# Performance work log

Measured on AMD Instinct MI355X. Metric: run time of the kernel, lower is better.

## Reference

```python
import jax, jax.numpy as jnp
import numpy as np

B, N, D = 64, 2048, 64
KC = 512
BETA = 0.5


def setup_inputs() -> dict:
    key = jax.random.key(0)
    k1, k2, k3 = jax.random.split(key, 3)
    F_active = jax.random.normal(k1, (B, N, D), dtype=jnp.float32)
    centers = jax.random.normal(k2, (KC, D), dtype=jnp.float32)
    psi = 0.1 * jax.random.normal(k3, (KC,), dtype=jnp.float32)
    beta = jnp.float32(BETA)
    return {"F_active": F_active, "centers": centers, "psi": psi, "beta": beta}


def reference(F_active, centers, psi, beta):
    # Squared Euclidean distance via GEMM expansion (avoids the (B,N,Kc,d) diff tensor):
    # ||f - c||^2 = ||f||^2 + ||c||^2 - 2 f.c
    f2 = jnp.sum(F_active * F_active, axis=-1, keepdims=True)          # (B, N, 1)
    c2 = jnp.sum(centers * centers, axis=-1)                           # (Kc,)
    fc = jnp.einsum('bnd,kd->bnk', F_active, centers)                  # (B, N, Kc)
    dist2 = jnp.maximum(f2 + c2[None, None, :] - 2.0 * fc, 0.0)       # (B, N, Kc)
    sim = jnp.exp(-beta * dist2)                                       # (B, N, Kc)
    w = jax.nn.softmax(psi, axis=0)                                    # (Kc,)
    score_per_slot = jnp.einsum('bnk,k->bn', sim, w)                   # (B, N)
    return jnp.mean(score_per_slot, axis=1)                            # (B,)
```

## Files before the change

### kernel.cpp

```cpp
#include <hip/hip_runtime.h>

typedef _Float16 f16x8 __attribute__((ext_vector_type(8)));
typedef float f32x4 __attribute__((ext_vector_type(4)));

static constexpr float kLog2e = 1.44269504088896340736f;

#define WS_E2 65536
#define WS_W  (65536 + 2048)
#define WS_SC (65536 + 4096)

__device__ __forceinline__ float fast_exp2(float x) {
#if __has_builtin(__builtin_amdgcn_exp2f)
  return __builtin_amdgcn_exp2f(x);
#else
  return exp2f(x);
#endif
}

__global__ __launch_bounds__(512) void prep_kernel(
    const float* __restrict__ centers, const float* __restrict__ psi,
    const float* __restrict__ beta, float* __restrict__ e2,
    float* __restrict__ w, float* __restrict__ sc) {
  __shared__ float red[8];
  const int tid = threadIdx.x;
  const int lane = tid & 63;
  const int wid = tid >> 6;
  const float b = beta[0];
  const float kco = -b * kLog2e;

  const float4* crow = (const float4*)(centers + tid * 64);
  float c2 = 0.f;
#pragma unroll
  for (int i = 0; i < 16; ++i) {
    const float4 v = crow[i];
    c2 = fmaf(v.x, v.x, c2); c2 = fmaf(v.y, v.y, c2);
    c2 = fmaf(v.z, v.z, c2); c2 = fmaf(v.w, v.w, c2);
  }

  const float p = psi[tid];
  float m = p;
#pragma unroll
  for (int d = 1; d < 64; d <<= 1) m = fmaxf(m, __shfl_xor(m, d, 64));
  if (lane == 0) red[wid] = m;
  __syncthreads();
  float mx = red[0];
#pragma unroll
  for (int i = 1; i < 8; ++i) mx = fmaxf(mx, red[i]);
  __syncthreads();
  const float ex = fast_exp2((p - mx) * kLog2e);
  float ssum = ex;
#pragma unroll
  for (int d = 1; d < 64; d <<= 1) ssum += __shfl_xor(ssum, d, 64);
  if (lane == 0) red[wid] = ssum;
  __syncthreads();
  float tot = 0.f;
#pragma unroll
  for (int i = 0; i < 8; ++i) tot += red[i];

  w[tid] = ex / tot;
  e2[tid] = kco * c2;
  if (tid == 0) { sc[0] = 2.f * b * kLog2e; sc[1] = kco; }
}

__global__ __launch_bounds__(64) void cfrag_kernel(
    const float* __restrict__ centers, _Float16* __restrict__ cfrag) {
  const int idx = blockIdx.x * 64 + threadIdx.x;
  const int lane = idx & 63;
  const int pair = idx >> 6;
  const int t = pair >> 1;
  const int kk = pair & 1;
  const int n = t * 16 + (lane & 15);
  const int k = kk * 32 + (lane >> 4) * 8;
  const float* src = centers + n * 64 + k;
  const float4 v0 = *(const float4*)(src);
  const float4 v1 = *(const float4*)(src + 4);
  f16x8 h;
  h[0] = (_Float16)v0.x; h[1] = (_Float16)v0.y;
  h[2] = (_Float16)v0.z; h[3] = (_Float16)v0.w;
  h[4] = (_Float16)v1.x; h[5] = (_Float16)v1.y;
  h[6] = (_Float16)v1.z; h[7] = (_Float16)v1.w;
  *(f16x8*)(cfrag + (size_t)idx * 8) = h;
}

__global__ __launch_bounds__(256, 4) void score_kernel(
    const float* __restrict__ F, const _Float16* __restrict__ cfrag,
    const float* __restrict__ e2, const float* __restrict__ wgt,
    const float* __restrict__ sc, float* __restrict__ out) {
  __shared__ float f2s[128];
  __shared__ float wsum[4];
  const int tid = threadIdx.x;
  const int lane = tid & 63;
  const int wv = tid >> 6;
  const int quad = lane >> 4;
  const int l15 = lane & 15;
  const int R0 = blockIdx.x * 128;

  const float cC = sc[0];
  const float kco = sc[1];

  f16x8 a[2][2];
#pragma unroll
  for (int rt = 0; rt < 2; ++rt) {
    const int row = R0 + wv * 32 + rt * 16 + l15;
    const float* fr = F + row * 64 + quad * 8;
    float ssq = 0.f;
#pragma unroll
    for (int kk = 0; kk < 2; ++kk) {
      const float4 v0 = *(const float4*)(fr + kk * 32);
      const float4 v1 = *(const float4*)(fr + kk * 32 + 4);
      a[rt][kk][0] = (_Float16)v0.x; a[rt][kk][1] = (_Float16)v0.y;
      a[rt][kk][2] = (_Float16)v0.z; a[rt][kk][3] = (_Float16)v0.w;
      a[rt][kk][4] = (_Float16)v1.x; a[rt][kk][5] = (_Float16)v1.y;
      a[rt][kk][6] = (_Float16)v1.z; a[rt][kk][7] = (_Float16)v1.w;
      ssq = fmaf(v0.x, v0.x, ssq); ssq = fmaf(v0.y, v0.y, ssq);
      ssq = fmaf(v0.z, v0.z, ssq); ssq = fmaf(v0.w, v0.w, ssq);
      ssq = fmaf(v1.x, v1.x, ssq); ssq = fmaf(v1.y, v1.y, ssq);
      ssq = fmaf(v1.z, v1.z, ssq); ssq = fmaf(v1.w, v1.w, ssq);
    }
    ssq += __shfl_xor(ssq, 16, 64);
    ssq += __shfl_xor(ssq, 32, 64);
    if (quad == 0) f2s[wv * 32 + rt * 16 + l15] = ssq;
  }
  __syncthreads();

  float p0[2][4];
#pragma unroll
  for (int rt = 0; rt < 2; ++rt)
#pragma unroll
    for (int r = 0; r < 4; ++r)
      p0[rt][r] = kco * f2s[wv * 32 + rt * 16 + quad * 4 + r];

  float s = 0.f;
  for (int t = 0; t < 32; ++t) {
    const f16x8 b0 = *(const f16x8*)(cfrag + (size_t)((t * 2 + 0) * 64 + lane) * 8);
    const f16x8 b1 = *(const f16x8*)(cfrag + (size_t)((t * 2 + 1) * 64 + lane) * 8);
    const float e2v = e2[t * 16 + l15];
    const float wv2 = wgt[t * 16 + l15];
    f32x4 acc0 = {0.f, 0.f, 0.f, 0.f};
    f32x4 acc1 = {0.f, 0.f, 0.f, 0.f};
    acc0 = __builtin_amdgcn_mfma_f32_16x16x32_f16(a[0][0], b0, acc0, 0, 0, 0);
    acc0 = __builtin_amdgcn_mfma_f32_16x16x32_f16(a[0][1], b1, acc0, 0, 0, 0);
    acc1 = __builtin_amdgcn_mfma_f32_16x16x32_f16(a[1][0], b0, acc1, 0, 0, 0);
    acc1 = __builtin_amdgcn_mfma_f32_16x16x32_f16(a[1][1], b1, acc1, 0, 0, 0);
    float esum = 0.f;
#pragma unroll
    for (int r = 0; r < 4; ++r) {
      const float arg0 = fminf(fmaf(acc0[r], cC, p0[0][r] + e2v), 0.f);
      const float arg1 = fminf(fmaf(acc1[r], cC, p0[1][r] + e2v), 0.f);
      esum += fast_exp2(arg0);
      esum += fast_exp2(arg1);
    }
    s = fmaf(wv2, esum, s);
  }

#pragma unroll
  for (int d = 1; d < 64; d <<= 1) s += __shfl_xor(s, d, 64);
  if (lane == 0) wsum[wv] = s;
  __syncthreads();
  if (tid == 0) {
    const float tot = wsum[0] + wsum[1] + wsum[2] + wsum[3];
    atomicAdd(out + (blockIdx.x >> 4), tot * (1.0f / 2048.0f));
  }
}

extern "C" void kernel_launch(void* const* d_in, const int* in_sizes, int n_in,
                              void* d_out, int out_size, void* d_ws, size_t ws_size,
                              hipStream_t stream) {
  const float* F = (const float*)d_in[0];
  const float* centers = (const float*)d_in[1];
  const float* psi = (const float*)d_in[2];
  const float* beta = (const float*)d_in[3];
  float* out = (float*)d_out;
  char* ws = (char*)d_ws;
  _Float16* cfrag = (_Float16*)ws;
  float* e2 = (float*)(ws + WS_E2);
  float* wgt = (float*)(ws + WS_W);
  float* sc = (float*)(ws + WS_SC);

  hipMemsetAsync(out, 0, out_size * sizeof(float), stream);
  prep_kernel<<<1, 512, 0, stream>>>(centers, psi, beta, e2, wgt, sc);
  cfrag_kernel<<<64, 64, 0, stream>>>(centers, cfrag);
  score_kernel<<<1024, 256, 0, stream>>>(F, cfrag, e2, wgt, sc, out);
}
```

Baseline: 104.3 us.

## Fuse prep, fragment and memset launches; fold bias and scale into MFMA

Folds the center fp16 fragment packing and the output zeroing into the single prep kernel. This removes a kernel launch and a memset. The score kernel now pre-scales F by 2*beta*log2e before the fp16 conversion and seeds the MFMA accumulator with the bias terms, which removes per-element FMAs from the exp loop. The e2 and weight values are packed into one float2 load, and the loop is unrolled by 2. Scaling before the fp16 cast slightly changes rounding, and the prep kernel's cfrag writes from a single block are less coalesced.

```diff
diff --git a/kernel.cpp b/kernel.cpp
--- a/kernel.cpp
+++ b/kernel.cpp
@@ -5,9 +5,7 @@
 
 static constexpr float kLog2e = 1.44269504088896340736f;
 
-#define WS_E2 65536
-#define WS_W  (65536 + 2048)
-#define WS_SC (65536 + 4096)
+#define WS_EW 65536
 
 __device__ __forceinline__ float fast_exp2(float x) {
 #if __has_builtin(__builtin_amdgcn_exp2f)
@@ -19,25 +17,26 @@
 
 __global__ __launch_bounds__(512) void prep_kernel(
     const float* __restrict__ centers, const float* __restrict__ psi,
-    const float* __restrict__ beta, float* __restrict__ e2,
-    float* __restrict__ w, float* __restrict__ sc) {
+    const float* __restrict__ beta, _Float16* __restrict__ cfrag,
+    float2* __restrict__ ew, float* __restrict__ out) {
   __shared__ float red[8];
-  const int tid = threadIdx.x;
-  const int lane = tid & 63;
-  const int wid = tid >> 6;
+  const int n = threadIdx.x;
+  const int lane = n & 63;
+  const int wid = n >> 6;
   const float b = beta[0];
   const float kco = -b * kLog2e;
 
-  const float4* crow = (const float4*)(centers + tid * 64);
+  float4 row[16];
+  const float4* crow = (const float4*)(centers + n * 64);
   float c2 = 0.f;
 #pragma unroll
   for (int i = 0; i < 16; ++i) {
-    const float4 v = crow[i];
-    c2 = fmaf(v.x, v.x, c2); c2 = fmaf(v.y, v.y, c2);
-    c2 = fmaf(v.z, v.z, c2); c2 = fmaf(v.w, v.w, c2);
+    row[i] = crow[i];
+    c2 = fmaf(row[i].x, row[i].x, c2); c2 = fmaf(row[i].y, row[i].y, c2);
+    c2 = fmaf(row[i].z, row[i].z, c2); c2 = fmaf(row[i].w, row[i].w, c2);
   }
 
-  const float p = psi[tid];
+  const float p = psi[n];
   float m = p;
 #pragma unroll
   for (int d = 1; d < 64; d <<= 1) m = fmaxf(m, __shfl_xor(m, d, 64));
@@ -57,35 +56,33 @@
 #pragma unroll
   for (int i = 0; i < 8; ++i) tot += red[i];
 
-  w[tid] = ex / tot;
-  e2[tid] = kco * c2;
-  if (tid == 0) { sc[0] = 2.f * b * kLog2e; sc[1] = kco; }
-}
+  ew[n] = make_float2(kco * c2, ex / tot);
 
-__global__ __launch_bounds__(64) void cfrag_kernel(
-    const float* __restrict__ centers, _Float16* __restrict__ cfrag) {
-  const int idx = blockIdx.x * 64 + threadIdx.x;
-  const int lane = idx & 63;
-  const int pair = idx >> 6;
-  const int t = pair >> 1;
-  const int kk = pair & 1;
-  const int n = t * 16 + (lane & 15);
-  const int k = kk * 32 + (lane >> 4) * 8;
-  const float* src = centers + n * 64 + k;
-  const float4 v0 = *(const float4*)(src);
-  const float4 v1 = *(const float4*)(src + 4);
-  f16x8 h;
-  h[0] = (_Float16)v0.x; h[1] = (_Float16)v0.y;
-  h[2] = (_Float16)v0.z; h[3] = (_Float16)v0.w;
-  h[4] = (_Float16)v1.x; h[5] = (_Float16)v1.y;
-  h[6] = (_Float16)v1.z; h[7] = (_Float16)v1.w;
-  *(f16x8*)(cfrag + (size_t)idx * 8) = h;
+  const int t = n >> 4;
+  const int l15 = n & 15;
+#pragma unroll
+  for (int kk = 0; kk < 2; ++kk) {
+#pragma unroll
+    for (int quad = 0; quad < 4; ++quad) {
+      const int idx = (t * 2 + kk) * 64 + quad * 16 + l15;
+      const float4 v0 = row[kk * 8 + quad * 2];
+      const float4 v1 = row[kk * 8 + quad * 2 + 1];
+      f16x8 h;
+      h[0] = (_Float16)v0.x; h[1] = (_Float16)v0.y;
+      h[2] = (_Float16)v0.z; h[3] = (_Float16)v0.w;
+      h[4] = (_Float16)v1.x; h[5] = (_Float16)v1.y;
+      h[6] = (_Float16)v1.z; h[7] = (_Float16)v1.w;
+      *(f16x8*)(cfrag + (size_t)idx * 8) = h;
+    }
+  }
+
+  if (n < 64) out[n] = 0.f;
 }
 
 __global__ __launch_bounds__(256, 4) void score_kernel(
     const float* __restrict__ F, const _Float16* __restrict__ cfrag,
-    const float* __restrict__ e2, const float* __restrict__ wgt,
-    const float* __restrict__ sc, float* __restrict__ out) {
+    const float2* __restrict__ ew, const float* __restrict__ beta,
+    float* __restrict__ out) {
   __shared__ float f2s[128];
   __shared__ float wsum[4];
   const int tid = threadIdx.x;
@@ -95,8 +92,9 @@
   const int l15 = lane & 15;
   const int R0 = blockIdx.x * 128;
 
-  const float cC = sc[0];
-  const float kco = sc[1];
+  const float b = beta[0];
+  const float cC = 2.f * b * kLog2e;
+  const float kco = -b * kLog2e;
 
   f16x8 a[2][2];
 #pragma unroll
@@ -108,14 +106,14 @@
     for (int kk = 0; kk < 2; ++kk) {
       const float4 v0 = *(const float4*)(fr + kk * 32);
       const float4 v1 = *(const float4*)(fr + kk * 32 + 4);
-      a[rt][kk][0] = (_Float16)v0.x; a[rt][kk][1] = (_Float16)v0.y;
-      a[rt][kk][2] = (_Float16)v0.z; a[rt][kk][3] = (_Float16)v0.w;
-      a[rt][kk][4] = (_Float16)v1.x; a[rt][kk][5] = (_Float16)v1.y;
-      a[rt][kk][6] = (_Float16)v1.z; a[rt][kk][7] = (_Float16)v1.w;
       ssq = fmaf(v0.x, v0.x, ssq); ssq = fmaf(v0.y, v0.y, ssq);
       ssq = fmaf(v0.z, v0.z, ssq); ssq = fmaf(v0.w, v0.w, ssq);
       ssq = fmaf(v1.x, v1.x, ssq); ssq = fmaf(v1.y, v1.y, ssq);
       ssq = fmaf(v1.z, v1.z, ssq); ssq = fmaf(v1.w, v1.w, ssq);
+      a[rt][kk][0] = (_Float16)(cC * v0.x); a[rt][kk][1] = (_Float16)(cC * v0.y);
+      a[rt][kk][2] = (_Float16)(cC * v0.z); a[rt][kk][3] = (_Float16)(cC * v0.w);
+      a[rt][kk][4] = (_Float16)(cC * v1.x); a[rt][kk][5] = (_Float16)(cC * v1.y);
+      a[rt][kk][6] = (_Float16)(cC * v1.z); a[rt][kk][7] = (_Float16)(cC * v1.w);
     }
     ssq += __shfl_xor(ssq, 16, 64);
     ssq += __shfl_xor(ssq, 32, 64);
@@ -131,13 +129,13 @@
       p0[rt][r] = kco * f2s[wv * 32 + rt * 16 + quad * 4 + r];
 
   float s = 0.f;
+#pragma unroll 2
   for (int t = 0; t < 32; ++t) {
     const f16x8 b0 = *(const f16x8*)(cfrag + (size_t)((t * 2 + 0) * 64 + lane) * 8);
     const f16x8 b1 = *(const f16x8*)(cfrag + (size_t)((t * 2 + 1) * 64 + lane) * 8);
-    const float e2v = e2[t * 16 + l15];
-    const float wv2 = wgt[t * 16 + l15];
-    f32x4 acc0 = {0.f, 0.f, 0.f, 0.f};
-    f32x4 acc1 = {0.f, 0.f, 0.f, 0.f};
+    const float2 ewv = ew[t * 16 + l15];
+    f32x4 acc0 = {p0[0][0] + ewv.x, p0[0][1] + ewv.x, p0[0][2] + ewv.x, p0[0][3] + ewv.x};
+    f32x4 acc1 = {p0[1][0] + ewv.x, p0[1][1] + ewv.x, p0[1][2] + ewv.x, p0[1][3] + ewv.x};
     acc0 = __builtin_amdgcn_mfma_f32_16x16x32_f16(a[0][0], b0, acc0, 0, 0, 0);
     acc0 = __builtin_amdgcn_mfma_f32_16x16x32_f16(a[0][1], b1, acc0, 0, 0, 0);
     acc1 = __builtin_amdgcn_mfma_f32_16x16x32_f16(a[1][0], b0, acc1, 0, 0, 0);
@@ -145,12 +143,10 @@
     float esum = 0.f;
 #pragma unroll
     for (int r = 0; r < 4; ++r) {
-      const float arg0 = fminf(fmaf(acc0[r], cC, p0[0][r] + e2v), 0.f);
-      const float arg1 = fminf(fmaf(acc1[r], cC, p0[1][r] + e2v), 0.f);
-      esum += fast_exp2(arg0);
-      esum += fast_exp2(arg1);
+      esum += fast_exp2(fminf(acc0[r], 0.f));
+      esum += fast_exp2(fminf(acc1[r], 0.f));
     }
-    s = fmaf(wv2, esum, s);
+    s = fmaf(ewv.y, esum, s);
   }
 
 #pragma unroll
@@ -173,12 +169,8 @@
   float* out = (float*)d_out;
   char* ws = (char*)d_ws;
   _Float16* cfrag = (_Float16*)ws;
-  float* e2 = (float*)(ws + WS_E2);
-  float* wgt = (float*)(ws + WS_W);
-  float* sc = (float*)(ws + WS_SC);
+  float2* ew = (float2*)(ws + WS_EW);
 
-  hipMemsetAsync(out, 0, out_size * sizeof(float), stream);
-  prep_kernel<<<1, 512, 0, stream>>>(centers, psi, beta, e2, wgt, sc);
-  cfrag_kernel<<<64, 64, 0, stream>>>(centers, cfrag);
-  score_kernel<<<1024, 256, 0, stream>>>(F, cfrag, e2, wgt, sc, out);
+  prep_kernel<<<1, 512, 0, stream>>>(centers, psi, beta, cfrag, ew, out);
+  score_kernel<<<1024, 256, 0, stream>>>(F, cfrag, ew, beta, out);
 }
```

Result: slower. 107.6 us (+3.2%).
